# Kernel optimization log

Measured on AMD Instinct MI355X. Metric: run time of the kernel, lower is better.

## Reference

```python
import jax, jax.numpy as jnp
import numpy as np

IOU_THRESHOLD = 0.5


def setup_inputs() -> dict:
    key = jax.random.key(0)
    k1, k2, k3 = jax.random.split(key, 3)
    B, N = 4, 8192
    # valid boxes: top-left in [0,200), width/height in [1,51)
    xy = jax.random.uniform(k1, (B, N, 2), dtype=jnp.float32) * 200.0
    wh = jax.random.uniform(k2, (B, N, 2), dtype=jnp.float32) * 50.0 + 1.0
    boxes = jnp.concatenate([xy, xy + wh], axis=-1)  # [B,N,4] (x1,y1,x2,y2)
    scores = jax.random.uniform(k3, (B, N), dtype=jnp.float32)
    return {"boxes": boxes, "scores": scores}


def _soft_nms_single(boxes, scores):
    # boxes: [N,4], scores: [N]
    x1, y1, x2, y2 = boxes[:, 0], boxes[:, 1], boxes[:, 2], boxes[:, 3]
    inter_w = jnp.maximum(0.0, jnp.minimum(x2[:, None], x2[None, :]) - jnp.maximum(x1[:, None], x1[None, :]))
    inter_h = jnp.maximum(0.0, jnp.minimum(y2[:, None], y2[None, :]) - jnp.maximum(y1[:, None], y1[None, :]))
    inter = inter_w * inter_h  # [N,N]
    area = (x2 - x1) * (y2 - y1)  # [N]
    union = area[:, None] + area[None, :] - inter
    iou = inter / union  # [N,N]
    weight = jnp.exp(-iou / IOU_THRESHOLD)  # [N,N]
    adjusted = weight @ scores  # [N] : adjusted_scores[i] = sum_j w[i,j]*s[j]
    w = jax.nn.softmax(adjusted, axis=0)  # [N]
    return w @ boxes  # [4]


def reference(boxes, scores):
    return jax.vmap(_soft_nms_single)(boxes, scores)  # [B,4]
```

## Files before the change

### kernel.cpp

```cpp
#include <hip/hip_runtime.h>
#include <hip/hip_bf16.h>

#define BATCH   4
#define NBOX    8192
#define BLOCK   256
#define TSZ     256
#define NT      (NBOX / TSZ)
#define NPAIRS  (NT * (NT + 1) / 2)
#define NBINS   2048
#define SUBS    8
#define SUBSZ   (NBOX / SUBS)

__device__ __forceinline__ float bf2f(unsigned short u) {
    union { unsigned int i; float f; } c;
    c.i = ((unsigned int)u) << 16;
    return c.f;
}

__device__ __forceinline__ bool box_plausible(float x1, float y1, float x2, float y2) {
    bool ok = (x1 == x1) && (y1 == y1) && (x2 == x2) && (y2 == y2);
    ok = ok && fabsf(x1) < 1e4f && fabsf(y1) < 1e4f && fabsf(x2) < 1e4f && fabsf(y2) < 1e4f;
    ok = ok && x1 >= -1.0f && x1 <= 300.0f && y1 >= -1.0f && y1 <= 300.0f;
    const float w = x2 - x1, h = y2 - y1;
    ok = ok && w >= -0.1f && w <= 80.0f && h >= -0.1f && h <= 80.0f;
    return ok;
}

__device__ __forceinline__ bool wave_probe_is_f32(const void* boxes_raw) {
    const int lane = threadIdx.x & 63;
    const float* bf = (const float*)boxes_raw;
    const bool okf = box_plausible(bf[lane * 4 + 0], bf[lane * 4 + 1],
                                   bf[lane * 4 + 2], bf[lane * 4 + 3]);
    const unsigned short* bh = (const unsigned short*)boxes_raw;
    const bool okh = box_plausible(bf2f(bh[lane * 4 + 0]), bf2f(bh[lane * 4 + 1]),
                                   bf2f(bh[lane * 4 + 2]), bf2f(bh[lane * 4 + 3]));
    const unsigned long long mf = __ballot(okf);
    const unsigned long long mh = __ballot(okh);
    return __popcll(mf) >= __popcll(mh);
}

__device__ __forceinline__ float4 load_box(const void* boxes_raw, size_t idx, bool isf32) {
    if (isf32) {
        return reinterpret_cast<const float4*>(boxes_raw)[idx];
    } else {
        const ushort4 u = reinterpret_cast<const ushort4*>(boxes_raw)[idx];
        return make_float4(bf2f(u.x), bf2f(u.y), bf2f(u.z), bf2f(u.w));
    }
}

__device__ __forceinline__ float load_score(const void* scores_raw, size_t idx, bool isf32) {
    return isf32 ? ((const float*)scores_raw)[idx]
                 : bf2f(((const unsigned short*)scores_raw)[idx]);
}

__device__ __forceinline__ int x1_bin(float x1) {
    const int bb = (int)(x1 * 8.0f);
    return min(NBINS - 1, max(0, bb));
}

#define CEXP (-2.8853900817779268f)

__device__ __forceinline__ float pair_weight(
    float ix1, float iy1, float ix2, float iy2, float iarea,
    const float4& bj, float jarea)
{
    float w = fminf(ix2, bj.z) - fmaxf(ix1, bj.x);
    float h = fminf(iy2, bj.w) - fmaxf(iy1, bj.y);
    w = fmaxf(w, 0.0f);
    h = fmaxf(h, 0.0f);
    const float inter = w * h;
    const float uni   = iarea + jarea - inter;
    const float arg   = (CEXP * inter) * __builtin_amdgcn_rcpf(uni);
    return __builtin_amdgcn_exp2f(arg);
}

__global__ __launch_bounds__(256) void hist_kernel(
    const void* __restrict__ boxes_raw,
    int* __restrict__ ghist,
    float* __restrict__ adj)
{
    __shared__ int hist[NBINS];
    const int b   = blockIdx.x / SUBS;
    const int sub = blockIdx.x % SUBS;
    const int tid = threadIdx.x;
    const bool isf32 = wave_probe_is_f32(boxes_raw);
    const size_t base = (size_t)b * NBOX;

    for (int i = tid; i < NBINS; i += 256) hist[i] = 0;
    {
        const size_t z = (size_t)blockIdx.x * 1024;
#pragma unroll
        for (int k = 0; k < 4; k++) adj[z + k * 256 + tid] = 0.0f;
    }
    __syncthreads();

#pragma unroll
    for (int k = 0; k < 4; k++) {
        const int i = sub * SUBSZ + k * 256 + tid;
        const float4 bx = load_box(boxes_raw, base + i, isf32);
        atomicAdd(&hist[x1_bin(bx.x)], 1);
    }
    __syncthreads();

    for (int i = tid; i < NBINS; i += 256)
        ghist[((size_t)b * NBINS + i) * SUBS + sub] = hist[i];
}

__global__ __launch_bounds__(256) void scatter_kernel(
    const void* __restrict__ boxes_raw, const void* __restrict__ scores_raw,
    const int* __restrict__ ghist,
    float4* __restrict__ sboxes, float* __restrict__ sscores,
    float* __restrict__ minx1c, float* __restrict__ maxx2c,
    int* __restrict__ pairlist, int* __restrict__ count)
{
    __shared__ int sex[NBINS];
    __shared__ int loff[NBINS];
    __shared__ int wsum[4];
    __shared__ float sminT[NT], smaxT[NT];
    __shared__ int scnt;

    const int b    = blockIdx.x / SUBS;
    const int sub  = blockIdx.x % SUBS;
    const int tid  = threadIdx.x;
    const int lane = tid & 63;
    const int wv   = tid >> 6;
    const bool isf32 = wave_probe_is_f32(boxes_raw);
    const size_t base = (size_t)b * NBOX;

    if (tid == 0) scnt = 0;

    int tot[8], mys[8], cum[8];
    {
        int run = 0;
#pragma unroll
        for (int i = 0; i < 8; i++) {
            const int bin = tid * 8 + i;
            const int* g = &ghist[((size_t)b * NBINS + bin) * SUBS];
            int t = 0, m = 0;
#pragma unroll
            for (int s = 0; s < SUBS; s++) {
                const int c = g[s];
                t += c;
                if (s < sub) m += c;
            }
            tot[i] = t; mys[i] = m;
            run += t; cum[i] = run;
        }
        int v = run;
#pragma unroll
        for (int d = 1; d < 64; d <<= 1) {
            const int u = __shfl_up(v, d);
            if (lane >= d) v += u;
        }
        if (lane == 63) wsum[wv] = v;
        __syncthreads();
        int wb = 0;
        for (int w = 0; w < wv; w++) wb += wsum[w];
        const int tb = wb + v - run;
#pragma unroll
        for (int i = 0; i < 8; i++) {
            const int e = tb + cum[i] - tot[i];
            sex[tid * 8 + i]  = e;
            loff[tid * 8 + i] = e + mys[i];
        }
    }
    __syncthreads();

    if (sub == 0 && tid < NT) {
        int p = tid * TSZ;
        int lo = 0, hi = NBINS - 1;
        while (lo < hi) { const int mid = (lo + hi + 1) >> 1;
                          if (sex[mid] <= p) lo = mid; else hi = mid - 1; }
        const int Bf = lo;
        p = tid * TSZ + TSZ - 1;
        lo = 0; hi = NBINS - 1;
        while (lo < hi) { const int mid = (lo + hi + 1) >> 1;
                          if (sex[mid] <= p) lo = mid; else hi = mid - 1; }
        const int Bl = lo;
        const float mn = (float)Bf * 0.125f;
        const float mx = (float)(Bl + 1) * 0.125f + 52.0f;
        sminT[tid] = mn; smaxT[tid] = mx;
        minx1c[b * NT + tid] = mn;
        maxx2c[b * NT + tid] = mx;
    }
    __syncthreads();

    if (sub == 0) {
        for (int q = tid; q < NPAIRS; q += 256) {
            int p = q, it = 0;
            while (p >= NT - it) { p -= NT - it; it++; }
            const int jt = it + p;
            const bool live = !((smaxT[it] < sminT[jt]) || (smaxT[jt] < sminT[it]));
            if (live) {
                const int idx = atomicAdd(&scnt, 1);
                pairlist[b * NPAIRS + idx] = (it << 8) | jt;
            }
        }
    }

#pragma unroll
    for (int k = 0; k < 4; k++) {
        const int i = sub * SUBSZ + k * 256 + tid;
        const float4 bx = load_box(boxes_raw, base + i, isf32);
        const float  sc = load_score(scores_raw, base + i, isf32);
        const int pos = atomicAdd(&loff[x1_bin(bx.x)], 1);
        sboxes[base + pos]  = bx;
        sscores[base + pos] = sc;
    }

    __syncthreads();
    if (sub == 0 && tid == 0) count[b] = scnt;
}

__global__ __launch_bounds__(BLOCK, 4) void soft_nms_adj_kernel(
    const float4* __restrict__ sboxes,
    const float* __restrict__ sscores,
    const int* __restrict__ pairlist,
    const int* __restrict__ count,
    float* __restrict__ adj)
{
    __shared__ float4 sbox[TSZ];
    __shared__ float2 sas[TSZ];
    __shared__ float  srow[4][TSZ];

    const int bid = blockIdx.x;
    const int b   = bid / NPAIRS;
    const int p   = bid % NPAIRS;
    if (p >= count[b]) return;
    const int pr = pairlist[b * NPAIRS + p];
    const int it = pr >> 8, jt = pr & 255;

    const int tid  = threadIdx.x;
    const int lane = tid & 63;
    const int wv   = tid >> 6;
    const size_t base = (size_t)b * NBOX;

    {
        const int jg = jt * TSZ + tid;
        const float4 uj = sboxes[base + jg];
        sbox[tid] = uj;
        sas[tid]  = make_float2((uj.z - uj.x) * (uj.w - uj.y), sscores[base + jg]);
    }

    float rx1[4], ry1[4], rx2[4], ry2[4], rar[4], rsc[4], accr[4];
#pragma unroll
    for (int k = 0; k < 4; k++) {
        const int ig = it * TSZ + k * 64 + lane;
        const float4 ui = sboxes[base + ig];
        rx1[k] = ui.x; ry1[k] = ui.y; rx2[k] = ui.z; ry2[k] = ui.w;
        rar[k] = (ui.z - ui.x) * (ui.w - ui.y);
        rsc[k] = sscores[base + ig];
        accr[k] = 0.0f;
    }

    __syncthreads();

    const int wvbase = wv * 64;

    if (it == jt) {
#pragma unroll 2
        for (int t = 0; t < 64; t++) {
            const int idx = wvbase + ((lane + t) & 63);
            const float4 bj = sbox[idx];
            const float2 as = sas[idx];
#pragma unroll
            for (int k = 0; k < 4; k++) {
                const float e = pair_weight(rx1[k], ry1[k], rx2[k], ry2[k], rar[k], bj, as.x);
                accr[k] = fmaf(e, as.y, accr[k]);
            }
        }
    } else {
        float accc = 0.0f;
#pragma unroll 2
        for (int t = 0; t < 64; t++) {
            const int idx = wvbase + ((lane + t) & 63);
            const float4 bj = sbox[idx];
            const float2 as = sas[idx];
            const float e0 = pair_weight(rx1[0], ry1[0], rx2[0], ry2[0], rar[0], bj, as.x);
            const float e1 = pair_weight(rx1[1], ry1[1], rx2[1], ry2[1], rar[1], bj, as.x);
            const float e2 = pair_weight(rx1[2], ry1[2], rx2[2], ry2[2], rar[2], bj, as.x);
            const float e3 = pair_weight(rx1[3], ry1[3], rx2[3], ry2[3], rar[3], bj, as.x);
            accr[0] = fmaf(e0, as.y, accr[0]);
            accr[1] = fmaf(e1, as.y, accr[1]);
            accr[2] = fmaf(e2, as.y, accr[2]);
            accr[3] = fmaf(e3, as.y, accr[3]);
            const float c = fmaf(e0, rsc[0], fmaf(e1, rsc[1], fmaf(e2, rsc[2], e3 * rsc[3])));
            accc += __shfl(c, (lane - t) & 63);
        }
        atomicAdd(&adj[base + jt * TSZ + wvbase + lane], accc);
    }

#pragma unroll
    for (int k = 0; k < 4; k++) srow[wv][k * 64 + lane] = accr[k];
    __syncthreads();
    {
        const float rs = srow[0][tid] + srow[1][tid] + srow[2][tid] + srow[3][tid];
        atomicAdd(&adj[base + it * TSZ + tid], rs);
    }
}

#define FBLK 1024
__global__ __launch_bounds__(FBLK) void soft_nms_finish_kernel(
    const float4* __restrict__ sboxes,
    const float* __restrict__ sscores,
    const float* __restrict__ adj,
    const float* __restrict__ minx1c, const float* __restrict__ maxx2c,
    const void* __restrict__ boxes_raw,
    void* __restrict__ out)
{
    constexpr int K  = NBOX / FBLK;
    constexpr int NW = FBLK / 64;
    __shared__ float sminx[NT], smaxx[NT], ssumT[NT], scorr[NT];
    __shared__ float smax_[NW];
    __shared__ float sred[NW][5];

    const int b    = blockIdx.x;
    const int tid  = threadIdx.x;
    const int lane = tid & 63;
    const int wv   = tid >> 6;
    const size_t base = (size_t)b * NBOX;

    const bool isf32 = wave_probe_is_f32(boxes_raw);

    if (tid < NT) {
        sminx[tid] = minx1c[b * NT + tid];
        smaxx[tid] = maxx2c[b * NT + tid];
    }
#pragma unroll
    for (int tt = 0; tt < 2; tt++) {
        const int T = wv * 2 + tt;
        float sm = 0.0f;
#pragma unroll
        for (int q = 0; q < 4; q++) sm += sscores[base + T * TSZ + q * 64 + lane];
#pragma unroll
        for (int off = 32; off > 0; off >>= 1) sm += __shfl_down(sm, off);
        if (lane == 0) ssumT[T] = sm;
    }
    __syncthreads();
    if (tid < NT) {
        float c = 0.0f;
        for (int T2 = 0; T2 < NT; T2++) {
            const bool skip = (smaxx[tid] < sminx[T2]) || (smaxx[T2] < sminx[tid]);
            if (skip) c += ssumT[T2];
        }
        scorr[tid] = c;
    }
    __syncthreads();

    float av[K];
    float m = -3.4e38f;
#pragma unroll
    for (int k = 0; k < K; k++) {
        const int r = k * FBLK + tid;
        av[k] = adj[base + r] + scorr[r >> 8];
        m = fmaxf(m, av[k]);
    }
#pragma unroll
    for (int off = 32; off > 0; off >>= 1)
        m = fmaxf(m, __shfl_down(m, off));
    if (lane == 0) smax_[wv] = m;
    __syncthreads();
    float M = smax_[0];
#pragma unroll
    for (int w = 1; w < NW; w++) M = fmaxf(M, smax_[w]);

    const float L2E = 1.4426950408889634f;
    float es = 0.0f, s0 = 0.0f, s1 = 0.0f, s2 = 0.0f, s3 = 0.0f;
#pragma unroll
    for (int k = 0; k < K; k++) {
        const float e = __builtin_amdgcn_exp2f((av[k] - M) * L2E);
        const float4 u = sboxes[base + k * FBLK + tid];
        es += e;
        s0 += e * u.x;
        s1 += e * u.y;
        s2 += e * u.z;
        s3 += e * u.w;
    }
#pragma unroll
    for (int off = 32; off > 0; off >>= 1) {
        es += __shfl_down(es, off);
        s0 += __shfl_down(s0, off);
        s1 += __shfl_down(s1, off);
        s2 += __shfl_down(s2, off);
        s3 += __shfl_down(s3, off);
    }
    if (lane == 0) {
        sred[wv][0] = es; sred[wv][1] = s0; sred[wv][2] = s1;
        sred[wv][3] = s2; sred[wv][4] = s3;
    }
    __syncthreads();
    if (tid == 0) {
        float ES = 0.0f, o[4] = {0.0f, 0.0f, 0.0f, 0.0f};
#pragma unroll
        for (int w = 0; w < NW; w++) {
            ES   += sred[w][0];
            o[0] += sred[w][1];
            o[1] += sred[w][2];
            o[2] += sred[w][3];
            o[3] += sred[w][4];
        }
        const float inv = 1.0f / ES;
        if (isf32) {
            float* of = (float*)out;
            for (int c = 0; c < 4; c++) of[b * 4 + c] = o[c] * inv;
        } else {
            __hip_bfloat16* oh = (__hip_bfloat16*)out;
            for (int c = 0; c < 4; c++) oh[b * 4 + c] = __float2bfloat16(o[c] * inv);
        }
    }
}

extern "C" void kernel_launch(void* const* d_in, const int* in_sizes, int n_in,
                              void* d_out, int out_size, void* d_ws, size_t ws_size,
                              hipStream_t stream) {
    const void* boxes_raw  = d_in[0];
    const void* scores_raw = d_in[1];

    char* w = (char*)d_ws;
    float4* sboxes   = (float4*)w;                 w += (size_t)BATCH * NBOX * 16;
    float*  sscores  = (float*)w;                  w += (size_t)BATCH * NBOX * 4;
    float*  adj      = (float*)w;                  w += (size_t)BATCH * NBOX * 4;
    int*    ghist    = (int*)w;                    w += (size_t)BATCH * NBINS * SUBS * 4;
    float*  minx1c   = (float*)w;                  w += (size_t)BATCH * NT * 4;
    float*  maxx2c   = (float*)w;                  w += (size_t)BATCH * NT * 4;
    int*    pairlist = (int*)w;                    w += (size_t)BATCH * NPAIRS * 4;
    int*    count    = (int*)w;

    hist_kernel<<<dim3(BATCH * SUBS), dim3(256), 0, stream>>>(boxes_raw, ghist, adj);
    scatter_kernel<<<dim3(BATCH * SUBS), dim3(256), 0, stream>>>(
        boxes_raw, scores_raw, ghist, sboxes, sscores, minx1c, maxx2c, pairlist, count);
    soft_nms_adj_kernel<<<dim3(BATCH * NPAIRS), dim3(BLOCK), 0, stream>>>(
        sboxes, sscores, pairlist, count, adj);
    soft_nms_finish_kernel<<<dim3(BATCH), dim3(FBLK), 0, stream>>>(
        sboxes, sscores, adj, minx1c, maxx2c, boxes_raw, d_out);
}
```

Measured before the change: 129.3 us.

## Fuse histogram and scatter into one sort kernel with exact tile x2 bounds

Merges the histogram and scatter kernels into a single 512-thread kernel in which each block redundantly builds the batch histogram and its own prefix histogram. This removes one kernel launch and the global histogram exchange. It also records the per-bin maximum x2 with an atomic max, so tile overlap bounds become exact rather than a fixed margin. Tighter bounds are meant to prune more tile pairs in the pairwise stage, at the cost of redundant box reads in every sort block.

```diff
diff --git a/kernel.cpp b/kernel.cpp
--- a/kernel.cpp
+++ b/kernel.cpp
@@ -10,6 +10,7 @@
 #define NBINS   2048
 #define SUBS    8
 #define SUBSZ   (NBOX / SUBS)
+#define STH     512
 
 __device__ __forceinline__ float bf2f(unsigned short u) {
     union { unsigned int i; float f; } c;
@@ -74,48 +75,17 @@
     return __builtin_amdgcn_exp2f(arg);
 }
 
-__global__ __launch_bounds__(256) void hist_kernel(
-    const void* __restrict__ boxes_raw,
-    int* __restrict__ ghist,
-    float* __restrict__ adj)
-{
-    __shared__ int hist[NBINS];
-    const int b   = blockIdx.x / SUBS;
-    const int sub = blockIdx.x % SUBS;
-    const int tid = threadIdx.x;
-    const bool isf32 = wave_probe_is_f32(boxes_raw);
-    const size_t base = (size_t)b * NBOX;
-
-    for (int i = tid; i < NBINS; i += 256) hist[i] = 0;
-    {
-        const size_t z = (size_t)blockIdx.x * 1024;
-#pragma unroll
-        for (int k = 0; k < 4; k++) adj[z + k * 256 + tid] = 0.0f;
-    }
-    __syncthreads();
-
-#pragma unroll
-    for (int k = 0; k < 4; k++) {
-        const int i = sub * SUBSZ + k * 256 + tid;
-        const float4 bx = load_box(boxes_raw, base + i, isf32);
-        atomicAdd(&hist[x1_bin(bx.x)], 1);
-    }
-    __syncthreads();
-
-    for (int i = tid; i < NBINS; i += 256)
-        ghist[((size_t)b * NBINS + i) * SUBS + sub] = hist[i];
-}
-
-__global__ __launch_bounds__(256) void scatter_kernel(
+__global__ __launch_bounds__(STH) void sort_kernel(
     const void* __restrict__ boxes_raw, const void* __restrict__ scores_raw,
-    const int* __restrict__ ghist,
     float4* __restrict__ sboxes, float* __restrict__ sscores,
+    float* __restrict__ adj,
     float* __restrict__ minx1c, float* __restrict__ maxx2c,
     int* __restrict__ pairlist, int* __restrict__ count)
 {
-    __shared__ int sex[NBINS];
-    __shared__ int loff[NBINS];
-    __shared__ int wsum[4];
+    __shared__ int hist[NBINS];
+    __shared__ int bmax[NBINS];
+    __shared__ int hist2[NBINS];
+    __shared__ int wsum[STH / 64];
     __shared__ float sminT[NT], smaxT[NT];
     __shared__ int scnt;
 
@@ -127,24 +97,40 @@
     const bool isf32 = wave_probe_is_f32(boxes_raw);
     const size_t base = (size_t)b * NBOX;
 
+#pragma unroll
+    for (int i = 0; i < NBINS / STH; i++) {
+        hist[i * STH + tid]  = 0;
+        bmax[i * STH + tid]  = 0;
+        hist2[i * STH + tid] = 0;
+    }
     if (tid == 0) scnt = 0;
-
-    int tot[8], mys[8], cum[8];
     {
+        const size_t z = (size_t)blockIdx.x * 1024;
+        adj[z + tid] = 0.0f;
+        adj[z + STH + tid] = 0.0f;
+    }
+    __syncthreads();
+
+#pragma unroll
+    for (int k = 0; k < NBOX / STH; k++) {
+        const float4 bx = load_box(boxes_raw, base + k * STH + tid, isf32);
+        const int bin = x1_bin(bx.x);
+        atomicAdd(&hist[bin], 1);
+        atomicMax(&bmax[bin], __float_as_int(bx.z));
+    }
+    for (int i = tid; i < sub * SUBSZ; i += STH) {
+        const float4 bx = load_box(boxes_raw, base + i, isf32);
+        atomicAdd(&hist2[x1_bin(bx.x)], 1);
+    }
+    __syncthreads();
+
+    {
+        int tot[4], cum[4];
         int run = 0;
 #pragma unroll
-        for (int i = 0; i < 8; i++) {
-            const int bin = tid * 8 + i;
-            const int* g = &ghist[((size_t)b * NBINS + bin) * SUBS];
-            int t = 0, m = 0;
-#pragma unroll
-            for (int s = 0; s < SUBS; s++) {
-                const int c = g[s];
-                t += c;
-                if (s < sub) m += c;
-            }
-            tot[i] = t; mys[i] = m;
-            run += t; cum[i] = run;
+        for (int i = 0; i < 4; i++) {
+            tot[i] = hist[tid * 4 + i];
+            run += tot[i]; cum[i] = run;
         }
         int v = run;
 #pragma unroll
@@ -158,35 +144,41 @@
         for (int w = 0; w < wv; w++) wb += wsum[w];
         const int tb = wb + v - run;
 #pragma unroll
-        for (int i = 0; i < 8; i++) {
+        for (int i = 0; i < 4; i++) {
+            const int bin = tid * 4 + i;
             const int e = tb + cum[i] - tot[i];
-            sex[tid * 8 + i]  = e;
-            loff[tid * 8 + i] = e + mys[i];
-        }
-    }
-    __syncthreads();
-
-    if (sub == 0 && tid < NT) {
+            const int m = hist2[bin];
+            hist[bin]  = e;
+            hist2[bin] = e + m;
+        }
+    }
+    __syncthreads();
+
+    if (tid < NT) {
         int p = tid * TSZ;
         int lo = 0, hi = NBINS - 1;
         while (lo < hi) { const int mid = (lo + hi + 1) >> 1;
-                          if (sex[mid] <= p) lo = mid; else hi = mid - 1; }
+                          if (hist[mid] <= p) lo = mid; else hi = mid - 1; }
         const int Bf = lo;
         p = tid * TSZ + TSZ - 1;
         lo = 0; hi = NBINS - 1;
         while (lo < hi) { const int mid = (lo + hi + 1) >> 1;
-                          if (sex[mid] <= p) lo = mid; else hi = mid - 1; }
+                          if (hist[mid] <= p) lo = mid; else hi = mid - 1; }
         const int Bl = lo;
+        int mb = 0;
+        for (int q = Bf; q <= Bl; q++) mb = max(mb, bmax[q]);
         const float mn = (float)Bf * 0.125f;
-        const float mx = (float)(Bl + 1) * 0.125f + 52.0f;
+        const float mx = __int_as_float(mb);
         sminT[tid] = mn; smaxT[tid] = mx;
-        minx1c[b * NT + tid] = mn;
-        maxx2c[b * NT + tid] = mx;
+        if (sub == 0) {
+            minx1c[b * NT + tid] = mn;
+            maxx2c[b * NT + tid] = mx;
+        }
     }
     __syncthreads();
 
     if (sub == 0) {
-        for (int q = tid; q < NPAIRS; q += 256) {
+        for (int q = tid; q < NPAIRS; q += STH) {
             int p = q, it = 0;
             while (p >= NT - it) { p -= NT - it; it++; }
             const int jt = it + p;
@@ -199,11 +191,11 @@
     }
 
 #pragma unroll
-    for (int k = 0; k < 4; k++) {
-        const int i = sub * SUBSZ + k * 256 + tid;
+    for (int k = 0; k < SUBSZ / STH; k++) {
+        const int i = sub * SUBSZ + k * STH + tid;
         const float4 bx = load_box(boxes_raw, base + i, isf32);
         const float  sc = load_score(scores_raw, base + i, isf32);
-        const int pos = atomicAdd(&loff[x1_bin(bx.x)], 1);
+        const int pos = atomicAdd(&hist2[x1_bin(bx.x)], 1);
         sboxes[base + pos]  = bx;
         sscores[base + pos] = sc;
     }
@@ -420,15 +412,13 @@
     float4* sboxes   = (float4*)w;                 w += (size_t)BATCH * NBOX * 16;
     float*  sscores  = (float*)w;                  w += (size_t)BATCH * NBOX * 4;
     float*  adj      = (float*)w;                  w += (size_t)BATCH * NBOX * 4;
-    int*    ghist    = (int*)w;                    w += (size_t)BATCH * NBINS * SUBS * 4;
     float*  minx1c   = (float*)w;                  w += (size_t)BATCH * NT * 4;
     float*  maxx2c   = (float*)w;                  w += (size_t)BATCH * NT * 4;
     int*    pairlist = (int*)w;                    w += (size_t)BATCH * NPAIRS * 4;
     int*    count    = (int*)w;
 
-    hist_kernel<<<dim3(BATCH * SUBS), dim3(256), 0, stream>>>(boxes_raw, ghist, adj);
-    scatter_kernel<<<dim3(BATCH * SUBS), dim3(256), 0, stream>>>(
-        boxes_raw, scores_raw, ghist, sboxes, sscores, minx1c, maxx2c, pairlist, count);
+    sort_kernel<<<dim3(BATCH * SUBS), dim3(STH), 0, stream>>>(
+        boxes_raw, scores_raw, sboxes, sscores, adj, minx1c, maxx2c, pairlist, count);
     soft_nms_adj_kernel<<<dim3(BATCH * NPAIRS), dim3(BLOCK), 0, stream>>>(
         sboxes, sscores, pairlist, count, adj);
     soft_nms_finish_kernel<<<dim3(BATCH), dim3(FBLK), 0, stream>>>(
```

Measured after the change: 120.8 us (median of 3 runs). 1.07x faster.
